# Optimization experiments

Measured on AMD Instinct MI355X. Metric: run time of the kernel, lower is better.

Reference implementation:

```python
import jax, jax.numpy as jnp
import numpy as np

EMBED_DIM = 64  # scale factor dim (matches head dim)


def setup_inputs() -> dict:
    key0 = jax.random.key(0)
    kq, kk, kv = jax.random.split(key0, 3)
    shape = (2, 16, 2048, 64)  # [B, H, S, D]
    return {
        "query": jax.random.normal(kq, shape, dtype=jnp.float32),
        "key": jax.random.normal(kk, shape, dtype=jnp.float32),
        "value": jax.random.normal(kv, shape, dtype=jnp.float32),
    }


def reference(query, key, value):
    # qk = Q K^T / sqrt(embed_dim); softmax over last dim; @ V
    inv_scale = jnp.sqrt(jnp.asarray(EMBED_DIM, dtype=query.dtype))
    scores = jnp.einsum("bhqd,bhkd->bhqk", query, key) / inv_scale
    probs = jax.nn.softmax(scores, axis=-1)
    # dropout_p=0.0 -> identity (eval semantics)
    return jnp.einsum("bhqk,bhkd->bhqd", probs, value)
```

## Files before the change

### kernel.cpp

```cpp
#include <hip/hip_runtime.h>
#include <hip/hip_bf16.h>

#define S_LEN 2048
#define DDIM  64
#define NT    (S_LEN / 64)
#define SCALE  0.125f
#define SCALE2 0.18033688f
#define NELEM  4194304
#define WC_LGKM0 0xc07f

typedef __attribute__((ext_vector_type(8))) short short8;
typedef __attribute__((ext_vector_type(4))) float floatx4;
typedef __attribute__((ext_vector_type(2))) float floatx2;
typedef __attribute__((ext_vector_type(2))) __bf16 bf16x2;

__device__ __forceinline__ short f2bf(float f) {
    union { float f; unsigned u; } v; v.f = f;
    return (short)((v.u + 0x7fffu + ((v.u >> 16) & 1u)) >> 16);
}

__device__ __forceinline__ unsigned pk2bf(float a, float b) {
    floatx2 f; f[0] = a; f[1] = b;
    bf16x2 h = __builtin_convertvector(f, bf16x2);
    union { bf16x2 v; unsigned u; } c; c.v = h; return c.u;
}

__device__ __forceinline__ float fexp2(float x) {
#if __has_builtin(__builtin_amdgcn_exp2f)
    return __builtin_amdgcn_exp2f(x);
#else
    return exp2f(x);
#endif
}

__device__ __forceinline__ void plswap32(unsigned &a, unsigned &b) {
    auto r = __builtin_amdgcn_permlane32_swap((int)a, (int)b, false, false);
    a = (unsigned)r[0]; b = (unsigned)r[1];
}
__device__ __forceinline__ void plswap16(unsigned &a, unsigned &b) {
    auto r = __builtin_amdgcn_permlane16_swap((int)a, (int)b, false, false);
    a = (unsigned)r[0]; b = (unsigned)r[1];
}

__global__ __launch_bounds__(256) void prep_v(const float* __restrict__ V,
                                              short* __restrict__ Vt) {
    const int bh = blockIdx.x & 31;
    const int st = blockIdx.x >> 5;
    const int t  = threadIdx.x;
    const size_t tile_off = (size_t)bh * (S_LEN * DDIM) + (size_t)st * (64 * DDIM);

    const int s4 = (t & 15) * 4;
    const int d4 = (t >> 4) * 4;
    const float* src = V + tile_off;
    float4 v0 = *(const float4*)(src + (size_t)(s4 + 0) * 64 + d4);
    float4 v1 = *(const float4*)(src + (size_t)(s4 + 1) * 64 + d4);
    float4 v2 = *(const float4*)(src + (size_t)(s4 + 2) * 64 + d4);
    float4 v3 = *(const float4*)(src + (size_t)(s4 + 3) * 64 + d4);
    const float* r0 = (const float*)&v0;
    const float* r1 = (const float*)&v1;
    const float* r2 = (const float*)&v2;
    const float* r3 = (const float*)&v3;
    short* dstb = Vt + (size_t)bh * (DDIM * S_LEN) + (size_t)st * 64 + s4;
    #pragma unroll
    for (int dd = 0; dd < 4; ++dd) {
        uint2 o;
        o.x = pk2bf(r0[dd], r1[dd]);
        o.y = pk2bf(r2[dd], r3[dd]);
        *(uint2*)(dstb + (size_t)(d4 + dd) * S_LEN) = o;
    }
}

__global__ __launch_bounds__(512) void attn_sm8(
    const float* __restrict__ Q, const float* __restrict__ K,
    const short* __restrict__ Vt, float* __restrict__ O)
{
    __shared__ short Ks[2][64 * 64];
    __shared__ short Vs[2][64 * 64];
    __shared__ float Dl[128];

    constexpr int NIT = NT / 2;

    const int tid  = threadIdx.x;
    const int wave = tid >> 6;
    const int grp  = wave >> 2;
    const int w4   = wave & 3;
    const int lane = tid & 63;
    const int l16  = lane & 15;
    const int quad = lane >> 4;
    const int x7   = l16 & 7;

    const int bh = blockIdx.x & 31;
    const int qt = blockIdx.x >> 5;
    const size_t base = (size_t)bh * (S_LEN * DDIM);

    const int g   = tid & 255;
    const int ci0 = g,        r0 = ci0 >> 3, c0 = (ci0 & 7) ^ (r0 & 7);
    const int ci1 = 256 + g,  r1 = ci1 >> 3, c1 = (ci1 & 7) ^ (r1 & 7);
    const size_t koff = (size_t)grp * NIT * (64 * 64);
    const size_t voff = (size_t)grp * NIT * 64;
    const float* pK0 = K  + base + koff + r0 * 64 + c0 * 8;
    const float* pK1 = K  + base + koff + r1 * 64 + c1 * 8;
    const short* pV0 = Vt + base + voff + (size_t)r0 * S_LEN + c0 * 8;
    const short* pV1 = Vt + base + voff + (size_t)r1 * S_LEN + c1 * 8;

    float4 ka0 = *(const float4*)(pK0);
    float4 ka1 = *(const float4*)(pK0 + 4);
    float4 kc0 = *(const float4*)(pK1);
    float4 kc1 = *(const float4*)(pK1 + 4);
    short8 rv0 = *(const short8*)pV0;
    short8 rv1 = *(const short8*)pV1;

    short8 qf[2][2];
    #pragma unroll
    for (int nq = 0; nq < 2; ++nq) {
        const float* qp = Q + base + (size_t)(qt * 128 + w4 * 32 + nq * 16 + l16) * 64 + quad * 8;
        #pragma unroll
        for (int kt = 0; kt < 2; ++kt) {
            float4 a = *(const float4*)(qp + kt * 32);
            float4 b = *(const float4*)(qp + kt * 32 + 4);
            union { unsigned u[4]; short8 s; } qc;
            qc.u[0] = pk2bf(a.x * SCALE2, a.y * SCALE2);
            qc.u[1] = pk2bf(a.z * SCALE2, a.w * SCALE2);
            qc.u[2] = pk2bf(b.x * SCALE2, b.y * SCALE2);
            qc.u[3] = pk2bf(b.z * SCALE2, b.w * SCALE2);
            qf[nq][kt] = qc.s;
        }
    }

    floatx4 oacc[2][4];
    float rs[2];
    #pragma unroll
    for (int mt = 0; mt < 2; ++mt) {
        #pragma unroll
        for (int dt = 0; dt < 4; ++dt) oacc[mt][dt] = (floatx4){0.f,0.f,0.f,0.f};
        rs[mt] = 0.f;
    }

    short* Ksg = &Ks[grp][0];
    short* Vsg = &Vs[grp][0];

    for (int kb = 0; kb < NIT; ++kb) {
        if (kb) __builtin_amdgcn_s_barrier();

        {
            uint4 ow0, ow1;
            ow0.x = pk2bf(ka0.x, ka0.y); ow0.y = pk2bf(ka0.z, ka0.w);
            ow0.z = pk2bf(ka1.x, ka1.y); ow0.w = pk2bf(ka1.z, ka1.w);
            ow1.x = pk2bf(kc0.x, kc0.y); ow1.y = pk2bf(kc0.z, kc0.w);
            ow1.z = pk2bf(kc1.x, kc1.y); ow1.w = pk2bf(kc1.z, kc1.w);
            *(uint4*)&Ksg[ci0 * 8] = ow0;
            *(uint4*)&Ksg[ci1 * 8] = ow1;
            *(short8*)&Vsg[ci0 * 8] = rv0;
            *(short8*)&Vsg[ci1 * 8] = rv1;
        }

        if (kb + 1 < NIT) {
            const int ok = (kb + 1) * (64 * 64), ov = (kb + 1) * 64;
            ka0 = *(const float4*)(pK0 + ok);
            ka1 = *(const float4*)(pK0 + ok + 4);
            kc0 = *(const float4*)(pK1 + ok);
            kc1 = *(const float4*)(pK1 + ok + 4);
            rv0 = *(const short8*)(pV0 + ov);
            rv1 = *(const short8*)(pV1 + ov);
        }

        __builtin_amdgcn_s_waitcnt(WC_LGKM0);
        __builtin_amdgcn_s_barrier();

        floatx4 sc[2][4];
        #pragma unroll
        for (int mk = 0; mk < 4; ++mk) {
            floatx4 a0 = (floatx4){0.f,0.f,0.f,0.f};
            floatx4 a1 = (floatx4){0.f,0.f,0.f,0.f};
            #pragma unroll
            for (int kt = 0; kt < 2; ++kt) {
                const int csw = (kt * 4 + quad) ^ x7;
                short8 kf = *(const short8*)&Ksg[(mk * 16 + l16) * 64 + csw * 8];
                a0 = __builtin_amdgcn_mfma_f32_16x16x32_bf16(kf, qf[0][kt], a0, 0, 0, 0);
                a1 = __builtin_amdgcn_mfma_f32_16x16x32_bf16(kf, qf[1][kt], a1, 0, 0, 0);
            }
            sc[0][mk] = a0; sc[1][mk] = a1;
        }

        unsigned pa[2][4], pb[2][4];
        #pragma unroll
        for (int nq = 0; nq < 2; ++nq) {
            #pragma unroll
            for (int mk = 0; mk < 4; ++mk) {
                float p0 = fexp2(sc[nq][mk][0]);
                float p1 = fexp2(sc[nq][mk][1]);
                float p2 = fexp2(sc[nq][mk][2]);
                float p3 = fexp2(sc[nq][mk][3]);
                rs[nq] += (p0 + p1) + (p2 + p3);
                pa[nq][mk] = pk2bf(p0, p1);
                pb[nq][mk] = pk2bf(p2, p3);
            }
        }

        #pragma unroll
        for (int kt = 0; kt < 2; ++kt) {
            short8 pf[2];
            #pragma unroll
            for (int nq = 0; nq < 2; ++nq) {
                unsigned a0 = pa[nq][2 * kt], a1 = pa[nq][2 * kt + 1];
                unsigned b0 = pb[nq][2 * kt], b1 = pb[nq][2 * kt + 1];
                plswap32(a0, a1); plswap16(a0, a1);
                plswap32(b0, b1); plswap16(b0, b1);
                union { unsigned u[4]; short8 s; } c;
                c.u[0] = a0; c.u[1] = b0; c.u[2] = a1; c.u[3] = b1;
                pf[nq] = c.s;
            }
            const int csw = (kt * 4 + quad) ^ x7;
            #pragma unroll
            for (int dt = 0; dt < 4; ++dt) {
                short8 vf = *(const short8*)&Vsg[(dt * 16 + l16) * 64 + csw * 8];
                oacc[0][dt] = __builtin_amdgcn_mfma_f32_16x16x32_bf16(pf[0], vf, oacc[0][dt], 0, 0, 0);
                oacc[1][dt] = __builtin_amdgcn_mfma_f32_16x16x32_bf16(pf[1], vf, oacc[1][dt], 0, 0, 0);
            }
        }
    }

    float sred[2];
    #pragma unroll
    for (int nq = 0; nq < 2; ++nq) {
        float s = rs[nq];
        s += __shfl_xor(s, 16, 64);
        s += __shfl_xor(s, 32, 64);
        sred[nq] = s;
    }

    if (grp == 1 && quad == 0) {
        Dl[w4 * 32 + l16]      = sred[0];
        Dl[w4 * 32 + 16 + l16] = sred[1];
    }
    __syncthreads();

    float invt[2];
    if (grp == 0) {
        invt[0] = 1.0f / (sred[0] + Dl[w4 * 32 + l16]);
        invt[1] = 1.0f / (sred[1] + Dl[w4 * 32 + 16 + l16]);
    }

    float* Nb = (float*)&Ks[0][0];
    #pragma unroll
    for (int mt = 0; mt < 2; ++mt) {
        if (grp == 1) {
            #pragma unroll
            for (int dt = 0; dt < 4; ++dt)
                #pragma unroll
                for (int r = 0; r < 4; ++r)
                    Nb[(dt * 4 + r) * 256 + w4 * 64 + lane] = oacc[mt][dt][r];
        }
        __syncthreads();
        if (grp == 0) {
            #pragma unroll
            for (int r = 0; r < 4; ++r) {
                const int row = qt * 128 + w4 * 32 + mt * 16 + quad * 4 + r;
                const float it = __shfl(invt[mt], quad * 4 + r, 64);
                float* op = O + base + (size_t)row * 64 + l16;
                #pragma unroll
                for (int dt = 0; dt < 4; ++dt)
                    op[dt * 16] = (oacc[mt][dt][r] + Nb[(dt * 4 + r) * 256 + w4 * 64 + lane]) * it;
            }
        }
        __syncthreads();
    }
}

#define BQ    64
#define BKEY  64
#define KPAD  72

__global__ __launch_bounds__(256) void attn_kernel(
    const float* __restrict__ Q, const float* __restrict__ K,
    const float* __restrict__ V, float* __restrict__ O)
{
    __shared__ short Ksh[BKEY * KPAD];
    __shared__ short Vtt[DDIM * KPAD];
    __shared__ short Pls[4][16 * KPAD];

    const int tid  = threadIdx.x;
    const int wave = tid >> 6;
    const int lane = tid & 63;
    const int l16  = lane & 15;
    const int quad = lane >> 4;

    const int bh = blockIdx.x & 31;
    const int qt = blockIdx.x >> 5;
    const size_t base = (size_t)bh * S_LEN * DDIM;

    const int qrow = qt * BQ + wave * 16 + l16;
    short8 qf[2];
    {
        const float* qp = Q + base + (size_t)qrow * DDIM + quad * 8;
        #pragma unroll
        for (int kt = 0; kt < 2; ++kt) {
            float4 a = *(const float4*)(qp + kt * 32);
            float4 b = *(const float4*)(qp + kt * 32 + 4);
            short* d = (short*)&qf[kt];
            d[0]=f2bf(a.x*SCALE); d[1]=f2bf(a.y*SCALE); d[2]=f2bf(a.z*SCALE); d[3]=f2bf(a.w*SCALE);
            d[4]=f2bf(b.x*SCALE); d[5]=f2bf(b.y*SCALE); d[6]=f2bf(b.z*SCALE); d[7]=f2bf(b.w*SCALE);
        }
    }
#undef SCALE

    float m_i[4], l_i[4];
    floatx4 oacc[4];
    #pragma unroll
    for (int r = 0; r < 4; ++r) { m_i[r] = -3.0e38f; l_i[r] = 0.f; }
    #pragma unroll
    for (int dt = 0; dt < 4; ++dt) oacc[dt] = (floatx4){0.f, 0.f, 0.f, 0.f};

    const int skey = tid >> 2;
    const int scol = (tid & 3) * 4;

    for (int kb = 0; kb < S_LEN / BKEY; ++kb) {
        const float* Kg = K + base + (size_t)kb * BKEY * DDIM + (size_t)skey * DDIM;
        const float* Vg = V + base + (size_t)kb * BKEY * DDIM + (size_t)skey * DDIM;
        #pragma unroll
        for (int i = 0; i < 4; ++i) {
            const int c = scol + i * 16;
            float4 kv = *(const float4*)(Kg + c);
            short* kd = &Ksh[skey * KPAD + c];
            kd[0]=f2bf(kv.x); kd[1]=f2bf(kv.y); kd[2]=f2bf(kv.z); kd[3]=f2bf(kv.w);
            float4 vv = *(const float4*)(Vg + c);
            Vtt[(c+0)*KPAD + skey] = f2bf(vv.x);
            Vtt[(c+1)*KPAD + skey] = f2bf(vv.y);
            Vtt[(c+2)*KPAD + skey] = f2bf(vv.z);
            Vtt[(c+3)*KPAD + skey] = f2bf(vv.w);
        }
        __syncthreads();

        floatx4 sc[4];
        #pragma unroll
        for (int nt = 0; nt < 4; ++nt) {
            floatx4 acc = (floatx4){0.f, 0.f, 0.f, 0.f};
            #pragma unroll
            for (int kt = 0; kt < 2; ++kt) {
                short8 kf = *(const short8*)&Ksh[(nt*16 + l16) * KPAD + kt*32 + quad*8];
                acc = __builtin_amdgcn_mfma_f32_16x16x32_bf16(qf[kt], kf, acc, 0, 0, 0);
            }
            sc[nt] = acc;
        }

        short* Pw = &Pls[wave][0];
        #pragma unroll
        for (int r = 0; r < 4; ++r) {
            float mx = fmaxf(fmaxf(sc[0][r], sc[1][r]), fmaxf(sc[2][r], sc[3][r]));
            #pragma unroll
            for (int off = 1; off < 16; off <<= 1)
                mx = fmaxf(mx, __shfl_xor(mx, off, 64));
            const float mnew  = fmaxf(m_i[r], mx);
            const float alpha = __expf(m_i[r] - mnew);
            m_i[r] = mnew;
            float rsum = 0.f;
            #pragma unroll
            for (int nt = 0; nt < 4; ++nt) {
                float p = __expf(sc[nt][r] - mnew);
                rsum += p;
                Pw[(quad*4 + r) * KPAD + nt*16 + l16] = f2bf(p);
            }
            #pragma unroll
            for (int off = 1; off < 16; off <<= 1)
                rsum += __shfl_xor(rsum, off, 64);
            l_i[r] = l_i[r] * alpha + rsum;
            oacc[0][r] *= alpha; oacc[1][r] *= alpha;
            oacc[2][r] *= alpha; oacc[3][r] *= alpha;
        }

        #pragma unroll
        for (int kt = 0; kt < 2; ++kt) {
            short8 pf = *(const short8*)&Pw[l16 * KPAD + kt*32 + quad*8];
            #pragma unroll
            for (int dt = 0; dt < 4; ++dt) {
                short8 vf = *(const short8*)&Vtt[(dt*16 + l16) * KPAD + kt*32 + quad*8];
                oacc[dt] = __builtin_amdgcn_mfma_f32_16x16x32_bf16(pf, vf, oacc[dt], 0, 0, 0);
            }
        }
        __syncthreads();
    }

    #pragma unroll
    for (int r = 0; r < 4; ++r) {
        const float inv = 1.0f / l_i[r];
        const int row = qt * BQ + wave * 16 + quad * 4 + r;
        float* op = O + base + (size_t)row * DDIM + l16;
        #pragma unroll
        for (int dt = 0; dt < 4; ++dt)
            op[dt * 16] = oacc[dt][r] * inv;
    }
}

extern "C" void kernel_launch(void* const* d_in, const int* in_sizes, int n_in,
                              void* d_out, int out_size, void* d_ws, size_t ws_size,
                              hipStream_t stream) {
    const float* Q = (const float*)d_in[0];
    const float* K = (const float*)d_in[1];
    const float* V = (const float*)d_in[2];
    float* O = (float*)d_out;

    const size_t prep_bytes = (size_t)NELEM * 2;

    if (ws_size >= prep_bytes) {
        short* Vtp = (short*)d_ws;
        prep_v<<<dim3(1024), dim3(256), 0, stream>>>(V, Vtp);
        attn_sm8<<<dim3(512), dim3(512), 0, stream>>>(Q, K, Vtp, O);
    } else {
        attn_kernel<<<dim3(1024), dim3(256), 0, stream>>>(Q, K, V, O);
    }
}
```

Before: 137.6 us.

## Halve queries per block to 64 and split final reduction across both groups

Each block now handles 64 query rows instead of 128, with each wave computing one 16-row tile, and the grid doubles to 1024 blocks. The intent is more parallelism and lower register pressure per wave. The cost is that K/V tiles are loaded and converted twice as often per query. The cross-group merge of the split-key partial results is also restructured so both groups exchange half of the output columns through shared memory, replacing the serial two-pass merge done by group 0.

```diff
diff --git a/kernel.cpp b/kernel.cpp
--- a/kernel.cpp
+++ b/kernel.cpp
@@ -70,13 +70,13 @@
     }
 }
 
-__global__ __launch_bounds__(512) void attn_sm8(
+__global__ __launch_bounds__(512) void attn_sm64(
     const float* __restrict__ Q, const float* __restrict__ K,
     const short* __restrict__ Vt, float* __restrict__ O)
 {
     __shared__ short Ks[2][64 * 64];
     __shared__ short Vs[2][64 * 64];
-    __shared__ float Dl[128];
+    __shared__ float Dl[2][64];
 
     constexpr int NIT = NT / 2;
 
@@ -110,10 +110,9 @@
     short8 rv0 = *(const short8*)pV0;
     short8 rv1 = *(const short8*)pV1;
 
-    short8 qf[2][2];
-    #pragma unroll
-    for (int nq = 0; nq < 2; ++nq) {
-        const float* qp = Q + base + (size_t)(qt * 128 + w4 * 32 + nq * 16 + l16) * 64 + quad * 8;
+    short8 qf[2];
+    {
+        const float* qp = Q + base + (size_t)(qt * 64 + w4 * 16 + l16) * 64 + quad * 8;
         #pragma unroll
         for (int kt = 0; kt < 2; ++kt) {
             float4 a = *(const float4*)(qp + kt * 32);
@@ -123,18 +122,14 @@
             qc.u[1] = pk2bf(a.z * SCALE2, a.w * SCALE2);
             qc.u[2] = pk2bf(b.x * SCALE2, b.y * SCALE2);
             qc.u[3] = pk2bf(b.z * SCALE2, b.w * SCALE2);
-            qf[nq][kt] = qc.s;
-        }
-    }
-
-    floatx4 oacc[2][4];
-    float rs[2];
-    #pragma unroll
-    for (int mt = 0; mt < 2; ++mt) {
-        #pragma unroll
-        for (int dt = 0; dt < 4; ++dt) oacc[mt][dt] = (floatx4){0.f,0.f,0.f,0.f};
-        rs[mt] = 0.f;
-    }
+            qf[kt] = qc.s;
+        }
+    }
+
+    floatx4 oacc[4];
+    float rs = 0.f;
+    #pragma unroll
+    for (int dt = 0; dt < 4; ++dt) oacc[dt] = (floatx4){0.f, 0.f, 0.f, 0.f};
 
     short* Ksg = &Ks[grp][0];
     short* Vsg = &Vs[grp][0];
@@ -167,103 +162,83 @@
         __builtin_amdgcn_s_waitcnt(WC_LGKM0);
         __builtin_amdgcn_s_barrier();
 
-        floatx4 sc[2][4];
+        floatx4 sc[4];
         #pragma unroll
         for (int mk = 0; mk < 4; ++mk) {
-            floatx4 a0 = (floatx4){0.f,0.f,0.f,0.f};
-            floatx4 a1 = (floatx4){0.f,0.f,0.f,0.f};
+            floatx4 a0 = (floatx4){0.f, 0.f, 0.f, 0.f};
             #pragma unroll
             for (int kt = 0; kt < 2; ++kt) {
                 const int csw = (kt * 4 + quad) ^ x7;
                 short8 kf = *(const short8*)&Ksg[(mk * 16 + l16) * 64 + csw * 8];
-                a0 = __builtin_amdgcn_mfma_f32_16x16x32_bf16(kf, qf[0][kt], a0, 0, 0, 0);
-                a1 = __builtin_amdgcn_mfma_f32_16x16x32_bf16(kf, qf[1][kt], a1, 0, 0, 0);
-            }
-            sc[0][mk] = a0; sc[1][mk] = a1;
-        }
-
-        unsigned pa[2][4], pb[2][4];
-        #pragma unroll
-        for (int nq = 0; nq < 2; ++nq) {
-            #pragma unroll
-            for (int mk = 0; mk < 4; ++mk) {
-                float p0 = fexp2(sc[nq][mk][0]);
-                float p1 = fexp2(sc[nq][mk][1]);
-                float p2 = fexp2(sc[nq][mk][2]);
-                float p3 = fexp2(sc[nq][mk][3]);
-                rs[nq] += (p0 + p1) + (p2 + p3);
-                pa[nq][mk] = pk2bf(p0, p1);
-                pb[nq][mk] = pk2bf(p2, p3);
-            }
+                a0 = __builtin_amdgcn_mfma_f32_16x16x32_bf16(kf, qf[kt], a0, 0, 0, 0);
+            }
+            sc[mk] = a0;
+        }
+
+        unsigned pa[4], pb[4];
+        #pragma unroll
+        for (int mk = 0; mk < 4; ++mk) {
+            float p0 = fexp2(sc[mk][0]);
+            float p1 = fexp2(sc[mk][1]);
+            float p2 = fexp2(sc[mk][2]);
+            float p3 = fexp2(sc[mk][3]);
+            rs += (p0 + p1) + (p2 + p3);
+            pa[mk] = pk2bf(p0, p1);
+            pb[mk] = pk2bf(p2, p3);
         }
 
         #pragma unroll
         for (int kt = 0; kt < 2; ++kt) {
-            short8 pf[2];
-            #pragma unroll
-            for (int nq = 0; nq < 2; ++nq) {
-                unsigned a0 = pa[nq][2 * kt], a1 = pa[nq][2 * kt + 1];
-                unsigned b0 = pb[nq][2 * kt], b1 = pb[nq][2 * kt + 1];
-                plswap32(a0, a1); plswap16(a0, a1);
-                plswap32(b0, b1); plswap16(b0, b1);
-                union { unsigned u[4]; short8 s; } c;
-                c.u[0] = a0; c.u[1] = b0; c.u[2] = a1; c.u[3] = b1;
-                pf[nq] = c.s;
-            }
+            unsigned a0 = pa[2 * kt], a1 = pa[2 * kt + 1];
+            unsigned b0 = pb[2 * kt], b1 = pb[2 * kt + 1];
+            plswap32(a0, a1); plswap16(a0, a1);
+            plswap32(b0, b1); plswap16(b0, b1);
+            union { unsigned u[4]; short8 s; } c;
+            c.u[0] = a0; c.u[1] = b0; c.u[2] = a1; c.u[3] = b1;
+            const short8 pf = c.s;
             const int csw = (kt * 4 + quad) ^ x7;
             #pragma unroll
             for (int dt = 0; dt < 4; ++dt) {
                 short8 vf = *(const short8*)&Vsg[(dt * 16 + l16) * 64 + csw * 8];
-                oacc[0][dt] = __builtin_amdgcn_mfma_f32_16x16x32_bf16(pf[0], vf, oacc[0][dt], 0, 0, 0);
-                oacc[1][dt] = __builtin_amdgcn_mfma_f32_16x16x32_bf16(pf[1], vf, oacc[1][dt], 0, 0, 0);
-            }
-        }
-    }
-
-    float sred[2];
-    #pragma unroll
-    for (int nq = 0; nq < 2; ++nq) {
-        float s = rs[nq];
-        s += __shfl_xor(s, 16, 64);
-        s += __shfl_xor(s, 32, 64);
-        sred[nq] = s;
-    }
-
-    if (grp == 1 && quad == 0) {
-        Dl[w4 * 32 + l16]      = sred[0];
-        Dl[w4 * 32 + 16 + l16] = sred[1];
-    }
+                oacc[dt] = __builtin_amdgcn_mfma_f32_16x16x32_bf16(pf, vf, oacc[dt], 0, 0, 0);
+            }
+        }
+    }
+
+    float sred = rs;
+    sred += __shfl_xor(sred, 16, 64);
+    sred += __shfl_xor(sred, 32, 64);
+
+    if (quad == 0) Dl[grp][w4 * 16 + l16] = sred;
     __syncthreads();
 
-    float invt[2];
-    if (grp == 0) {
-        invt[0] = 1.0f / (sred[0] + Dl[w4 * 32 + l16]);
-        invt[1] = 1.0f / (sred[1] + Dl[w4 * 32 + 16 + l16]);
-    }
-
-    float* Nb = (float*)&Ks[0][0];
-    #pragma unroll
-    for (int mt = 0; mt < 2; ++mt) {
-        if (grp == 1) {
-            #pragma unroll
-            for (int dt = 0; dt < 4; ++dt)
-                #pragma unroll
-                for (int r = 0; r < 4; ++r)
-                    Nb[(dt * 4 + r) * 256 + w4 * 64 + lane] = oacc[mt][dt][r];
-        }
-        __syncthreads();
-        if (grp == 0) {
-            #pragma unroll
-            for (int r = 0; r < 4; ++r) {
-                const int row = qt * 128 + w4 * 32 + mt * 16 + quad * 4 + r;
-                const float it = __shfl(invt[mt], quad * 4 + r, 64);
-                float* op = O + base + (size_t)row * 64 + l16;
-                #pragma unroll
-                for (int dt = 0; dt < 4; ++dt)
-                    op[dt * 16] = (oacc[mt][dt][r] + Nb[(dt * 4 + r) * 256 + w4 * 64 + lane]) * it;
-            }
-        }
-        __syncthreads();
+    const float invc = 1.0f / (sred + Dl[1 - grp][w4 * 16 + l16]);
+
+    {
+        float* NbMine = (float*)&Ks[grp][0];
+        #pragma unroll
+        for (int dtl = 0; dtl < 2; ++dtl) {
+            const int dtp = (1 - grp) * 2 + dtl;
+            #pragma unroll
+            for (int r = 0; r < 4; ++r)
+                NbMine[(dtl * 4 + r) * 256 + w4 * 64 + lane] = oacc[dtp][r];
+        }
+    }
+    __syncthreads();
+
+    {
+        const float* NbOther = (const float*)&Ks[1 - grp][0];
+        #pragma unroll
+        for (int r = 0; r < 4; ++r) {
+            const int row = qt * 64 + w4 * 16 + quad * 4 + r;
+            const float it = __shfl(invc, quad * 4 + r, 64);
+            float* op = O + base + (size_t)row * 64 + l16;
+            #pragma unroll
+            for (int dtl = 0; dtl < 2; ++dtl) {
+                const int dts = grp * 2 + dtl;
+                op[dts * 16] = (oacc[dts][r] + NbOther[(dtl * 4 + r) * 256 + w4 * 64 + lane]) * it;
+            }
+        }
     }
 }
 
@@ -302,7 +277,6 @@
             d[4]=f2bf(b.x*SCALE); d[5]=f2bf(b.y*SCALE); d[6]=f2bf(b.z*SCALE); d[7]=f2bf(b.w*SCALE);
         }
     }
-#undef SCALE
 
     float m_i[4], l_i[4];
     floatx4 oacc[4];
@@ -404,7 +378,7 @@
     if (ws_size >= prep_bytes) {
         short* Vtp = (short*)d_ws;
         prep_v<<<dim3(1024), dim3(256), 0, stream>>>(V, Vtp);
-        attn_sm8<<<dim3(512), dim3(512), 0, stream>>>(Q, K, Vtp, O);
+        attn_sm64<<<dim3(1024), dim3(512), 0, stream>>>(Q, K, Vtp, O);
     } else {
         attn_kernel<<<dim3(1024), dim3(256), 0, stream>>>(Q, K, V, O);
     }
```

Result: slower. 145.1 us (+5.4%).
